# Kernel tuning notes

Hardware: AMD Instinct MI355X
Metric: run time of the kernel (lower is better)

Reference implementation:

```python
import jax, jax.numpy as jnp
import numpy as np

B, C, H, W = 4, 1024, 64, 64


def setup_inputs() -> dict:
    key = jax.random.key(0)
    x = jax.random.normal(key, (B, C, H, W), dtype=jnp.float32)
    return {"x": x}


def reference(x) -> jnp.ndarray:
    b, c, h, w = x.shape
    n = b * h * w  # total non-channel elements
    x_nc = x.reshape(-1, c)          # (N, C)  row-major flatten, same as torch reshape
    x_cn = x.reshape(c, -1)          # (C, N)
    attn = jax.nn.softmax(x_cn @ x_nc, axis=-1)   # (C, C) GEMM + softmax
    out = jax.nn.softmax(attn @ x_cn, axis=-1)    # (C, N) GEMM + softmax over N
    y = out.reshape(b, c, h, w)
    return x + jax.nn.softmax(y, axis=-1)          # softmax over W, residual add
```

## Files before the change

kernel.cpp:

```cpp
#include <hip/hip_runtime.h>
#include <hip/hip_bf16.h>


typedef __bf16 bf16x8 __attribute__((ext_vector_type(8)));
typedef float f32x4 __attribute__((ext_vector_type(4)));
typedef unsigned short u16;
typedef unsigned short u16x4 __attribute__((ext_vector_type(4)));
typedef unsigned short u16x8 __attribute__((ext_vector_type(8)));

#define DEV __device__ __forceinline__

DEV float bf2f(u16 u) { return __uint_as_float(((unsigned int)u) << 16); }
DEV u16 f2bf(float f) {
  unsigned int x = __float_as_uint(f);
  return (u16)((x + 0x7FFFu + ((x >> 16) & 1u)) >> 16);
}

DEV void gld16(const u16* g, u16* lds) {
  __builtin_amdgcn_global_load_lds(
      (const __attribute__((address_space(1))) unsigned int*)g,
      (__attribute__((address_space(3))) unsigned int*)lds, 16, 0, 0);
}

__global__ __launch_bounds__(256) void cast_f32_bf16(const float* __restrict__ in,
                                                     u16* __restrict__ out) {
  int i = (blockIdx.x * 256 + threadIdx.x) * 4;
  float4 v = *reinterpret_cast<const float4*>(in + i);
  u16x4 o;
  o[0] = f2bf(v.x); o[1] = f2bf(v.y); o[2] = f2bf(v.z); o[3] = f2bf(v.w);
  *reinterpret_cast<u16x4*>(out + i) = o;
}

__global__ __launch_bounds__(256) void transpose_cast(const float* __restrict__ in,
                                                      u16* __restrict__ out,
                                                      int R, int C) {
  __shared__ float tile[32][33];
  const int c0 = blockIdx.x * 32, r0 = blockIdx.y * 32;
  const int tx = threadIdx.x, ty = threadIdx.y;
#pragma unroll
  for (int j = 0; j < 4; ++j)
    tile[ty + j * 8][tx] = in[(size_t)(r0 + ty + j * 8) * C + c0 + tx];
  __syncthreads();
#pragma unroll
  for (int j = 0; j < 4; ++j)
    out[(size_t)(c0 + ty + j * 8) * R + r0 + tx] = f2bf(tile[tx][ty + j * 8]);
}


#define FENCE() asm volatile("" ::: "memory")
#define BAR()                           \
  {                                     \
    FENCE();                            \
    __builtin_amdgcn_s_barrier();       \
    __builtin_amdgcn_sched_barrier(0);  \
    FENCE();                            \
  }
#define LGKM0()                                          \
  {                                                      \
    asm volatile("s_waitcnt lgkmcnt(0)" ::: "memory");   \
    __builtin_amdgcn_sched_barrier(0);                   \
  }

#define DS_A(BUF, H, MG)                                        \
  {                                                             \
    const u16* Ab_ = &lds[(BUF)][0][(H)][0] + aoff + (MG)*2048; \
    a[0] = *(const bf16x8*)(Ab_);                               \
    a[1] = *(const bf16x8*)(Ab_ + 512);                         \
    a[2] = *(const bf16x8*)(Ab_ + 1024);                        \
    a[3] = *(const bf16x8*)(Ab_ + 1536);                        \
  }
#define DS_B(BUF, H)                                            \
  {                                                             \
    const u16* Bb_ = &lds[(BUF)][1][(H)][0] + boff;             \
    b[0] = *(const bf16x8*)(Bb_);                               \
    b[1] = *(const bf16x8*)(Bb_ + 512);                         \
    b[2] = *(const bf16x8*)(Bb_ + 1024);                        \
    b[3] = *(const bf16x8*)(Bb_ + 1536);                        \
  }
#define STAGE(BUF, MAT, H, KCOL, P, LD)        \
  {                                            \
    u16* d_ = &lds[(BUF)][(MAT)][(H)][0];      \
    gld16((P) + (KCOL), d_ + wb0);             \
    gld16((P) + (KCOL) + (LD), d_ + wb1);      \
  }
#define MMA(MG)                                                              \
  {                                                                          \
    __builtin_amdgcn_s_setprio(1);                                           \
    _Pragma("unroll") for (int i_ = 0; i_ < 4; ++i_) {                       \
      _Pragma("unroll") for (int n_ = 0; n_ < 4; ++n_)                       \
        acc[(MG)*4 + i_][n_] = __builtin_amdgcn_mfma_f32_16x16x32_bf16(      \
            a[i_], b[n_], acc[(MG)*4 + i_][n_], 0, 0, 0);                    \
    }                                                                        \
    __builtin_amdgcn_s_setprio(0);                                           \
  }

#define TILE(BC, BN, T, DO_S12, DO_S34, W2, W4)                      \
  {                                                                  \
                                                  \
    DS_A((BC), 0, 0); DS_B((BC), 0);                                 \
    if (DO_S12) STAGE((BN), 0, 1, ((T) + 1) * 64 + 32, pA, ldA128);  \
    BAR(); LGKM0(); MMA(0); BAR();                                   \
                                                  \
    DS_A((BC), 0, 1);                                                \
    if (DO_S12) STAGE((BN), 1, 1, ((T) + 1) * 64 + 32, pB, ldB128);  \
    asm volatile("s_waitcnt vmcnt(" #W2 ")" ::: "memory");           \
    BAR(); LGKM0(); MMA(1); BAR();                                   \
                                                  \
    DS_A((BC), 1, 0); DS_B((BC), 1);                                 \
    if (DO_S34) STAGE((BC), 0, 0, ((T) + 2) * 64, pA, ldA128);       \
    BAR(); LGKM0(); MMA(0); BAR();                                   \
                                                  \
    DS_A((BC), 1, 1);                                                \
    if (DO_S34) STAGE((BC), 1, 0, ((T) + 2) * 64, pB, ldB128);       \
    asm volatile("s_waitcnt vmcnt(" #W4 ")" ::: "memory");           \
    BAR(); LGKM0(); MMA(1); BAR();                                   \
  }

template <int MODE>
__global__ __launch_bounds__(512, 2) void gemm256(const u16* __restrict__ A,
                                                  const u16* __restrict__ Bt,
                                                  u16* __restrict__ C,
                                                  int lda, int ldbt, int ldc,
                                                  long zstride) {
  __shared__ __align__(16) u16 lds[2][2][2][8192];

  const int tid = threadIdx.x;
  const int w = tid >> 6, l = tid & 63;
  const int wr = w >> 2, wc = w & 3;

  const int hw = blockIdx.x;
  const int logical = ((hw & 7) << 5) | (hw >> 3);
  int bx, by, z;
  if (MODE == 0) { bx = logical & 3; by = (logical >> 2) & 3; z = logical >> 4; }
  else           { by = logical & 3; bx = logical >> 2;       z = 0; }
  const int brow = by * 256, bcol = bx * 256;
  const int kbase = z << 10;

  const int srow = w * 16 + (l >> 2);
  const int swz = (((l & 3) ^ ((l >> 2) & 3) ^ ((l >> 4) & 1)) * 8);
  const u16* pA = A + (size_t)(brow + srow) * lda + kbase + swz;
  const u16* pB = Bt + (size_t)(bcol + srow) * ldbt + kbase + swz;
  const size_t ldA128 = (size_t)128 * lda, ldB128 = (size_t)128 * ldbt;
  const int wb0 = (w * 16) * 32, wb1 = (w * 16 + 128) * 32;

  const int slotp = (l >> 4) ^ (l & 3) ^ ((l >> 2) & 1);
  const int aoff = (wr * 128 + (l & 15)) * 32 + slotp * 8;
  const int boff = (wc * 64 + (l & 15)) * 32 + slotp * 8;

  STAGE(0, 0, 0, 0, pA, ldA128);
  STAGE(0, 1, 0, 0, pB, ldB128);
  STAGE(0, 0, 1, 32, pA, ldA128);
  STAGE(0, 1, 1, 32, pB, ldB128);
  STAGE(1, 0, 0, 64, pA, ldA128);
  STAGE(1, 1, 0, 64, pB, ldB128);

  f32x4 acc[8][4];
#pragma unroll
  for (int m = 0; m < 8; ++m)
#pragma unroll
    for (int n = 0; n < 4; ++n) acc[m][n] = f32x4{0.f, 0.f, 0.f, 0.f};

  bf16x8 a[4], b[4];

  asm volatile("s_waitcnt vmcnt(8)" ::: "memory");
  BAR();

#pragma unroll 1
  for (int t = 0; t < 14; ++t) {
    const int bc = t & 1;
    TILE(bc, bc ^ 1, t, 1, 1, 8, 8);
  }
  TILE(0, 1, 14, 1, 0, 8, 4);
  TILE(1, 0, 15, 0, 0, 0, 0);

  u16* Cz = C + (size_t)z * zstride;
  const int er = brow + wr * 128 + ((l >> 4) << 2);
  const int ec = bcol + wc * 64 + (l & 15);
#pragma unroll
  for (int m = 0; m < 8; ++m)
#pragma unroll
    for (int n = 0; n < 4; ++n)
#pragma unroll
      for (int j = 0; j < 4; ++j)
        Cz[(size_t)(er + m * 16 + j) * ldc + ec + n * 16] = f2bf(acc[m][n][j]);
}

__global__ __launch_bounds__(256) void softmax1(const u16* __restrict__ Sp,
                                                u16* __restrict__ attn) {
  const int row = blockIdx.x, t = threadIdx.x;
  float s0 = 0.f, s1 = 0.f, s2 = 0.f, s3 = 0.f;
#pragma unroll
  for (int z = 0; z < 16; ++z) {
    u16x4 v = *reinterpret_cast<const u16x4*>(Sp + (size_t)z * 1024 * 1024 +
                                              (size_t)row * 1024 + t * 4);
    s0 += bf2f(v[0]); s1 += bf2f(v[1]); s2 += bf2f(v[2]); s3 += bf2f(v[3]);
  }
  __shared__ float red[256];
  red[t] = fmaxf(fmaxf(s0, s1), fmaxf(s2, s3));
  __syncthreads();
  for (int off = 128; off > 0; off >>= 1) {
    if (t < off) red[t] = fmaxf(red[t], red[t + off]);
    __syncthreads();
  }
  const float rowmax = red[0];
  __syncthreads();
  float e0 = __expf(s0 - rowmax), e1 = __expf(s1 - rowmax);
  float e2 = __expf(s2 - rowmax), e3 = __expf(s3 - rowmax);
  red[t] = e0 + e1 + e2 + e3;
  __syncthreads();
  for (int off = 128; off > 0; off >>= 1) {
    if (t < off) red[t] += red[t + off];
    __syncthreads();
  }
  const float inv = 1.0f / red[0];
  u16x4 o;
  o[0] = f2bf(e0 * inv); o[1] = f2bf(e1 * inv);
  o[2] = f2bf(e2 * inv); o[3] = f2bf(e3 * inv);
  *reinterpret_cast<u16x4*>(attn + (size_t)row * 1024 + t * 4) = o;
}

__global__ __launch_bounds__(1024) void softmax2(const u16* __restrict__ Sc,
                                                 u16* __restrict__ Y) {
  const int row = blockIdx.x, t = threadIdx.x;
  const size_t base = (size_t)row * 16384 + (size_t)t * 16;
  u16x8 u0 = *reinterpret_cast<const u16x8*>(Sc + base);
  u16x8 u1 = *reinterpret_cast<const u16x8*>(Sc + base + 8);
  float v[16];
#pragma unroll
  for (int j = 0; j < 8; ++j) { v[j] = bf2f(u0[j]); v[8 + j] = bf2f(u1[j]); }
  float m = v[0];
#pragma unroll
  for (int j = 1; j < 16; ++j) m = fmaxf(m, v[j]);
  __shared__ float red[1024];
  red[t] = m;
  __syncthreads();
  for (int off = 512; off > 0; off >>= 1) {
    if (t < off) red[t] = fmaxf(red[t], red[t + off]);
    __syncthreads();
  }
  const float rowmax = red[0];
  __syncthreads();
  float e[16], sum = 0.f;
#pragma unroll
  for (int j = 0; j < 16; ++j) { e[j] = __expf(v[j] - rowmax); sum += e[j]; }
  red[t] = sum;
  __syncthreads();
  for (int off = 512; off > 0; off >>= 1) {
    if (t < off) red[t] += red[t + off];
    __syncthreads();
  }
  const float inv = 1.0f / red[0];
  u16x8 o0, o1;
#pragma unroll
  for (int j = 0; j < 8; ++j) { o0[j] = f2bf(e[j] * inv); o1[j] = f2bf(e[8 + j] * inv); }
  *reinterpret_cast<u16x8*>(Y + base) = o0;
  *reinterpret_cast<u16x8*>(Y + base + 8) = o1;
}

__global__ __launch_bounds__(256) void final_softmax_add(const u16* __restrict__ Y,
                                                         const float* __restrict__ X,
                                                         float* __restrict__ O) {
  const int i = blockIdx.x * 256 + threadIdx.x;
  const float y = bf2f(Y[i]);
  float m = y;
#pragma unroll
  for (int off = 32; off > 0; off >>= 1) m = fmaxf(m, __shfl_xor(m, off, 64));
  const float e = __expf(y - m);
  float s = e;
#pragma unroll
  for (int off = 32; off > 0; off >>= 1) s += __shfl_xor(s, off, 64);
  O[i] = X[i] + e / s;
}

extern "C" void kernel_launch(void* const* d_in, const int* in_sizes, int n_in,
                              void* d_out, int out_size, void* d_ws, size_t ws_size,
                              hipStream_t stream) {
  const float* x = (const float*)d_in[0];
  float* out = (float*)d_out;
  char* ws = (char*)d_ws;

  const size_t MiB = 1u << 20;
  if (ws_size < 98 * MiB) return;
  u16* A16 = (u16*)(ws);
  u16* Bt1 = (u16*)(ws + 32 * MiB);
  u16* Sp16 = (u16*)(ws + 64 * MiB);
  u16* attn = (u16*)(ws + 96 * MiB);
  u16* Sc = A16;
  u16* Y = Sp16;

  cast_f32_bf16<<<16384, 256, 0, stream>>>(x, A16);
  transpose_cast<<<dim3(32, 512), dim3(32, 8), 0, stream>>>(x, Bt1, 16384, 1024);
  gemm256<0><<<256, 512, 0, stream>>>(A16, Bt1, Sp16, 16384, 16384, 1024,
                                      (long)1024 * 1024);
  softmax1<<<1024, 256, 0, stream>>>(Sp16, attn);
  transpose_cast<<<dim3(512, 32), dim3(32, 8), 0, stream>>>(x, Bt1, 1024, 16384);
  gemm256<1><<<256, 512, 0, stream>>>(attn, Bt1, Sc, 1024, 1024, 16384, 0);
  softmax2<<<1024, 1024, 0, stream>>>(Sc, Y);
  final_softmax_add<<<65536, 256, 0, stream>>>(Y, x, out);
}
```

Baseline: 276.2 us.

## Fuse input cast with transpose, reuse bf16 copy, fold final softmax into softmax2

Merges the f32→bf16 cast and the first transpose into one kernel that reads x once and writes both layouts. The second transpose now reads the bf16 copy instead of re-reading f32 x. The last W-softmax and residual add are folded into the N-softmax kernel: each 64-wide W segment spans four adjacent threads and is reduced with shuffles. This removes one pass over x and a bf16 round trip of Y through memory, and drops two launches. In exchange the final softmax now runs on full-precision values rather than bf16-rounded Y, which slightly changes numerics.

```diff
diff --git a/kernel.cpp b/kernel.cpp
--- a/kernel.cpp
+++ b/kernel.cpp
@@ -22,28 +22,37 @@
       (__attribute__((address_space(3))) unsigned int*)lds, 16, 0, 0);
 }
 
-__global__ __launch_bounds__(256) void cast_f32_bf16(const float* __restrict__ in,
-                                                     u16* __restrict__ out) {
-  int i = (blockIdx.x * 256 + threadIdx.x) * 4;
-  float4 v = *reinterpret_cast<const float4*>(in + i);
-  u16x4 o;
-  o[0] = f2bf(v.x); o[1] = f2bf(v.y); o[2] = f2bf(v.z); o[3] = f2bf(v.w);
-  *reinterpret_cast<u16x4*>(out + i) = o;
-}
-
-__global__ __launch_bounds__(256) void transpose_cast(const float* __restrict__ in,
-                                                      u16* __restrict__ out,
-                                                      int R, int C) {
-  __shared__ float tile[32][33];
-  const int c0 = blockIdx.x * 32, r0 = blockIdx.y * 32;
+__global__ __launch_bounds__(512) void prep_t1(const float* __restrict__ x,
+                                               u16* __restrict__ A16,
+                                               u16* __restrict__ Bt1) {
+  __shared__ float tile[64][65];
+  const int c0 = blockIdx.x * 64, r0 = blockIdx.y * 64;
   const int tx = threadIdx.x, ty = threadIdx.y;
 #pragma unroll
-  for (int j = 0; j < 4; ++j)
-    tile[ty + j * 8][tx] = in[(size_t)(r0 + ty + j * 8) * C + c0 + tx];
-  __syncthreads();
-#pragma unroll
-  for (int j = 0; j < 4; ++j)
-    out[(size_t)(c0 + ty + j * 8) * R + r0 + tx] = f2bf(tile[tx][ty + j * 8]);
+  for (int j = 0; j < 8; ++j) {
+    const size_t idx = (size_t)(r0 + ty + j * 8) * 1024 + c0 + tx;
+    float v = x[idx];
+    tile[ty + j * 8][tx] = v;
+    A16[idx] = f2bf(v);
+  }
+  __syncthreads();
+#pragma unroll
+  for (int j = 0; j < 8; ++j)
+    Bt1[(size_t)(c0 + ty + j * 8) * 16384 + r0 + tx] = f2bf(tile[tx][ty + j * 8]);
+}
+
+__global__ __launch_bounds__(512) void t2_bf16(const u16* __restrict__ in,
+                                               u16* __restrict__ out) {
+  __shared__ u16 tile[64][68];
+  const int c0 = blockIdx.x * 64, r0 = blockIdx.y * 64;
+  const int tx = threadIdx.x, ty = threadIdx.y;
+#pragma unroll
+  for (int j = 0; j < 8; ++j)
+    tile[ty + j * 8][tx] = in[(size_t)(r0 + ty + j * 8) * 16384 + c0 + tx];
+  __syncthreads();
+#pragma unroll
+  for (int j = 0; j < 8; ++j)
+    out[(size_t)(c0 + ty + j * 8) * 1024 + r0 + tx] = tile[tx][ty + j * 8];
 }
 
 
@@ -96,20 +105,16 @@
 
 #define TILE(BC, BN, T, DO_S12, DO_S34, W2, W4)                      \
   {                                                                  \
-                                                  \
     DS_A((BC), 0, 0); DS_B((BC), 0);                                 \
     if (DO_S12) STAGE((BN), 0, 1, ((T) + 1) * 64 + 32, pA, ldA128);  \
     BAR(); LGKM0(); MMA(0); BAR();                                   \
-                                                  \
     DS_A((BC), 0, 1);                                                \
     if (DO_S12) STAGE((BN), 1, 1, ((T) + 1) * 64 + 32, pB, ldB128);  \
     asm volatile("s_waitcnt vmcnt(" #W2 ")" ::: "memory");           \
     BAR(); LGKM0(); MMA(1); BAR();                                   \
-                                                  \
     DS_A((BC), 1, 0); DS_B((BC), 1);                                 \
     if (DO_S34) STAGE((BC), 0, 0, ((T) + 2) * 64, pA, ldA128);       \
     BAR(); LGKM0(); MMA(0); BAR();                                   \
-                                                  \
     DS_A((BC), 1, 1);                                                \
     if (DO_S34) STAGE((BC), 1, 0, ((T) + 2) * 64, pB, ldB128);       \
     asm volatile("s_waitcnt vmcnt(" #W4 ")" ::: "memory");           \
@@ -219,8 +224,9 @@
   *reinterpret_cast<u16x4*>(attn + (size_t)row * 1024 + t * 4) = o;
 }
 
-__global__ __launch_bounds__(1024) void softmax2(const u16* __restrict__ Sc,
-                                                 u16* __restrict__ Y) {
+__global__ __launch_bounds__(1024) void softmax2_final(const u16* __restrict__ Sc,
+                                                       const float* __restrict__ X,
+                                                       float* __restrict__ O) {
   const int row = blockIdx.x, t = threadIdx.x;
   const size_t base = (size_t)row * 16384 + (size_t)t * 16;
   u16x8 u0 = *reinterpret_cast<const u16x8*>(Sc + base);
@@ -250,26 +256,31 @@
     __syncthreads();
   }
   const float inv = 1.0f / red[0];
-  u16x8 o0, o1;
-#pragma unroll
-  for (int j = 0; j < 8; ++j) { o0[j] = f2bf(e[j] * inv); o1[j] = f2bf(e[8 + j] * inv); }
-  *reinterpret_cast<u16x8*>(Y + base) = o0;
-  *reinterpret_cast<u16x8*>(Y + base + 8) = o1;
-}
-
-__global__ __launch_bounds__(256) void final_softmax_add(const u16* __restrict__ Y,
-                                                         const float* __restrict__ X,
-                                                         float* __restrict__ O) {
-  const int i = blockIdx.x * 256 + threadIdx.x;
-  const float y = bf2f(Y[i]);
-  float m = y;
-#pragma unroll
-  for (int off = 32; off > 0; off >>= 1) m = fmaxf(m, __shfl_xor(m, off, 64));
-  const float e = __expf(y - m);
-  float s = e;
-#pragma unroll
-  for (int off = 32; off > 0; off >>= 1) s += __shfl_xor(s, off, 64);
-  O[i] = X[i] + e / s;
+
+  float em = e[0];
+#pragma unroll
+  for (int j = 1; j < 16; ++j) em = fmaxf(em, e[j]);
+  em = fmaxf(em, __shfl_xor(em, 1, 64));
+  em = fmaxf(em, __shfl_xor(em, 2, 64));
+  const float ym = em * inv;
+
+  float eg[16], sg = 0.f;
+#pragma unroll
+  for (int j = 0; j < 16; ++j) { eg[j] = __expf(e[j] * inv - ym); sg += eg[j]; }
+  sg += __shfl_xor(sg, 1, 64);
+  sg += __shfl_xor(sg, 2, 64);
+  const float inv2 = 1.0f / sg;
+
+#pragma unroll
+  for (int q = 0; q < 4; ++q) {
+    float4 xv = *reinterpret_cast<const float4*>(X + base + q * 4);
+    float4 o;
+    o.x = xv.x + eg[q * 4 + 0] * inv2;
+    o.y = xv.y + eg[q * 4 + 1] * inv2;
+    o.z = xv.z + eg[q * 4 + 2] * inv2;
+    o.w = xv.w + eg[q * 4 + 3] * inv2;
+    *reinterpret_cast<float4*>(O + base + q * 4) = o;
+  }
 }
 
 extern "C" void kernel_launch(void* const* d_in, const int* in_sizes, int n_in,
@@ -282,19 +293,16 @@
   const size_t MiB = 1u << 20;
   if (ws_size < 98 * MiB) return;
   u16* A16 = (u16*)(ws);
-  u16* Bt1 = (u16*)(ws + 32 * MiB);
+  u16* Bt = (u16*)(ws + 32 * MiB);
   u16* Sp16 = (u16*)(ws + 64 * MiB);
   u16* attn = (u16*)(ws + 96 * MiB);
   u16* Sc = A16;
-  u16* Y = Sp16;
-
-  cast_f32_bf16<<<16384, 256, 0, stream>>>(x, A16);
-  transpose_cast<<<dim3(32, 512), dim3(32, 8), 0, stream>>>(x, Bt1, 16384, 1024);
-  gemm256<0><<<256, 512, 0, stream>>>(A16, Bt1, Sp16, 16384, 16384, 1024,
+
+  prep_t1<<<dim3(16, 256), dim3(64, 8), 0, stream>>>(x, A16, Bt);
+  gemm256<0><<<256, 512, 0, stream>>>(A16, Bt, Sp16, 16384, 16384, 1024,
                                       (long)1024 * 1024);
   softmax1<<<1024, 256, 0, stream>>>(Sp16, attn);
-  transpose_cast<<<dim3(512, 32), dim3(32, 8), 0, stream>>>(x, Bt1, 1024, 16384);
-  gemm256<1><<<256, 512, 0, stream>>>(attn, Bt1, Sc, 1024, 1024, 16384, 0);
-  softmax2<<<1024, 1024, 0, stream>>>(Sc, Y);
-  final_softmax_add<<<65536, 256, 0, stream>>>(Y, x, out);
-}
+  t2_bf16<<<dim3(256, 16), dim3(64, 8), 0, stream>>>(A16, Bt);
+  gemm256<1><<<256, 512, 0, stream>>>(attn, Bt, Sc, 1024, 1024, 16384, 0);
+  softmax2_final<<<1024, 1024, 0, stream>>>(Sc, x, out);
+}
```

Result: faster. 236.9 us (-14.2%).
